# Kernel optimization log

Hardware: AMD Instinct MI355X
Metric: run time of the kernel (lower is better)

Reference implementation:

```python
import jax, jax.numpy as jnp
import numpy as np

# Supernet configuration (matches init_kwargs)
HIDDEN = [1024, 2048]
HEADS = [8, 16]
ABITS = [4, 8]
WBITS = [4, 8]
B, S = 4, 4096
MAX_IN = max(HIDDEN)            # 2048
MAX_OUT = max(HIDDEN)           # min(heads)*max(hidden)//min(heads) = 2048


def fake_quant(v, s, bit):
    """LSQ-style symmetric fake quantization with straight-through rounding."""
    qp = float(2 ** (bit - 1) - 1)
    qn = -float(2 ** (bit - 1))
    vs = jnp.clip(v / s, qn, qp)
    vq = vs + jax.lax.stop_gradient(jnp.round(vs) - vs)  # STE round
    return vq * s


def setup_inputs() -> dict:
    key = jax.random.key(0)
    k1, k2, k3, k4 = jax.random.split(key, 4)
    x = jax.random.normal(k1, (B, S, MAX_IN), jnp.float32)
    weights = jax.random.uniform(k2, (16,), jnp.float32)  # arch mixing coeffs
    W = jax.random.normal(k3, (MAX_OUT, MAX_IN), jnp.float32) * 0.02
    b = jax.random.normal(k4, (MAX_OUT,), jnp.float32) * 0.02
    # init_weight_scale: LSQ init 2*mean(|W|)/sqrt(Qp) per weight bitwidth
    w_scales = jnp.stack([2.0 * jnp.mean(jnp.abs(W)) / jnp.sqrt(float(2 ** (bit - 1) - 1))
                          for bit in WBITS])
    a_scales = jnp.ones((len(ABITS),), jnp.float32)
    return {"x": x, "weights": weights, "W": W, "b": b,
            "a_scales": a_scales, "w_scales": w_scales}


def reference(x, weights, W, b, a_scales, w_scales):
    # Non-argmax mixture path (reverse=False):
    # for each (hidden_i, heads_j, abit_m, wbit_n): slice W to
    # [out_dim, in_dim], zero-pad to [MAX_OUT, MAX_IN] (== masking, since
    # per-tensor fake-quant maps 0 -> 0), quantize, and weighted-accumulate.
    # Quantized x / W depend only on abit / wbit, so compute each once.
    qx = [fake_quant(x, a_scales[m], ABITS[m]) for m in range(len(ABITS))]   # [B,S,MAX_IN]
    qw = [fake_quant(W, w_scales[n], WBITS[n]) for n in range(len(WBITS))]  # [MAX_OUT,MAX_IN]
    out_idx = jnp.arange(MAX_OUT)
    in_idx = jnp.arange(MAX_IN)

    w_mix = jnp.zeros_like(W)
    x_mix = jnp.zeros_like(x)
    b_mix = jnp.zeros_like(b)
    k = 0
    for i, h in enumerate(HIDDEN):
        for j, nh in enumerate(HEADS):
            head_dim = h // nh
            out_dim = nh * head_dim  # == h when divisible
            in_dim = h
            wmask = (out_idx[:, None] < out_dim) & (in_idx[None, :] < in_dim)
            bmask = out_idx < out_dim
            for m in range(len(ABITS)):
                for n in range(len(WBITS)):
                    a = weights[k]
                    w_mix = w_mix + a * jnp.where(wmask, qw[n], 0.0)
                    x_mix = x_mix + a * qx[m]
                    b_mix = b_mix + a * jnp.where(bmask, b, 0.0)
                    k += 1
    # out = F.linear(x_mix, w_mix, b_mix)
    out = jnp.einsum('bsi,oi->bso', x_mix, w_mix) + b_mix
    return out
```

## Files before the change

### kernel.cpp

```cpp
#include <hip/hip_runtime.h>
#include <hip/hip_bf16.h>
#include <stdint.h>

#define MDIM 16384
#define NDIM 2048
#define KDIM 2048

typedef __attribute__((ext_vector_type(4))) float f32x4;
typedef __attribute__((ext_vector_type(8))) short s16x8;

__device__ __forceinline__ void gload_lds16(const __hip_bfloat16* g, void* l) {
    __builtin_amdgcn_global_load_lds(
        (const __attribute__((address_space(1))) void*)g,
        (__attribute__((address_space(3))) void*)l,
        16, 0, 0);
}

#define XBLKS 16384
#define WBLKS 2048

__global__ __launch_bounds__(256) void prep_all(
    const float* __restrict__ x, const float* __restrict__ weights,
    const float* __restrict__ W, const float* __restrict__ b,
    const float* __restrict__ a_scales, const float* __restrict__ w_scales,
    __hip_bfloat16* __restrict__ xq, __hip_bfloat16* __restrict__ wq,
    float* __restrict__ bm)
{
    const int blk = blockIdx.x;
    if (blk < XBLKS) {
        float A0 = 0.f, A1 = 0.f;
        #pragma unroll
        for (int k = 0; k < 16; ++k) {
            float w = weights[k];
            if (((k >> 1) & 1) == 0) A0 += w; else A1 += w;
        }
        const float s0 = a_scales[0], s1 = a_scales[1];
        const float r0 = 1.f / s0, r1 = 1.f / s1;

        size_t idx = ((size_t)blk * 256 + threadIdx.x) * 8;
        const f32x4* xv = (const f32x4*)(x + idx);
        f32x4 v0 = xv[0], v1 = xv[1];
        float vals[8] = {v0.x, v0.y, v0.z, v0.w, v1.x, v1.y, v1.z, v1.w};

        union { s16x8 v; __hip_bfloat16 h[8]; } u;
        #pragma unroll
        for (int j = 0; j < 8; ++j) {
            float q0 = rintf(fminf(fmaxf(vals[j] * r0, -8.f),   7.f)) * s0;
            float q1 = rintf(fminf(fmaxf(vals[j] * r1, -128.f), 127.f)) * s1;
            u.h[j] = __float2bfloat16(A0 * q0 + A1 * q1);
        }
        *(s16x8*)(xq + idx) = u.v;
    } else if (blk < XBLKS + WBLKS) {
        float c00 = weights[0] + weights[2]  + weights[4]  + weights[6];
        float c01 = weights[1] + weights[3]  + weights[5]  + weights[7];
        float c10 = weights[8] + weights[10] + weights[12] + weights[14];
        float c11 = weights[9] + weights[11] + weights[13] + weights[15];

        const float s0 = w_scales[0], s1 = w_scales[1];
        const float r0 = 1.f / s0, r1 = 1.f / s1;

        size_t idx = ((size_t)(blk - XBLKS) * 256 + threadIdx.x) * 8;
        const int o = (int)(idx >> 11);
        const int c = (int)(idx & 2047);
        const bool inner = (o < 1024) && (c < 1024);
        const float k0 = inner ? (c00 + c10) : c10;
        const float k1 = inner ? (c01 + c11) : c11;

        const f32x4* wv = (const f32x4*)(W + idx);
        f32x4 v0 = wv[0], v1 = wv[1];
        float vals[8] = {v0.x, v0.y, v0.z, v0.w, v1.x, v1.y, v1.z, v1.w};

        union { s16x8 v; __hip_bfloat16 h[8]; } u;
        #pragma unroll
        for (int j = 0; j < 8; ++j) {
            float q0 = rintf(fminf(fmaxf(vals[j] * r0, -8.f),   7.f)) * s0;
            float q1 = rintf(fminf(fmaxf(vals[j] * r1, -128.f), 127.f)) * s1;
            u.h[j] = __float2bfloat16(k0 * q0 + k1 * q1);
        }
        *(s16x8*)(wq + idx) = u.v;
    } else {
        int o = (blk - XBLKS - WBLKS) * 256 + threadIdx.x;
        if (o < NDIM) {
            float S1 = 0.f, S0 = 0.f;
            #pragma unroll
            for (int k = 0; k < 8; ++k)  S0 += weights[k];
            #pragma unroll
            for (int k = 8; k < 16; ++k) S1 += weights[k];
            bm[o] = b[o] * ((o < 1024) ? (S0 + S1) : S1);
        }
    }
}


#define NCH 64
#define ASLOT 16384
#define BREG  65536

#define MFMA(a, b, c) __builtin_amdgcn_mfma_f32_16x16x32_bf16((a), (b), (c), 0, 0, 0)

#define CHUNK(S, T)                                                          \
  {                                                                          \
    asm volatile("" ::: "memory");      \
    s16x8 af[8], bf[4];                                                      \
    _Pragma("unroll")                                                        \
    for (int m_ = 0; m_ < 8; ++m_)                                           \
      af[m_] = *(const s16x8*)(lds + (S) * ASLOT + aoff + m_ * 1024);        \
    _Pragma("unroll")                                                        \
    for (int n_ = 0; n_ < 4; ++n_)                                           \
      bf[n_] = *(const s16x8*)(lds + BREG + (S) * ASLOT + boff + n_ * 1024); \
    gload_lds16(As0 + kg * 32, lds + (T) * ASLOT + ldoff);                   \
    gload_lds16(As1 + kg * 32, lds + (T) * ASLOT + 8192 + ldoff);            \
    gload_lds16(Bs0 + kg * 32, lds + BREG + (T) * ASLOT + ldoff);            \
    gload_lds16(Bs1 + kg * 32, lds + BREG + (T) * ASLOT + 8192 + ldoff);     \
    kg = (kg + 1) & (NCH - 1);                                               \
    __builtin_amdgcn_s_setprio(1);                                           \
    _Pragma("unroll")                                                        \
    for (int m_ = 0; m_ < 8; ++m_) {                                         \
      acc[m_][0] = MFMA(af[m_], bf[0], acc[m_][0]);                          \
      acc[m_][1] = MFMA(af[m_], bf[1], acc[m_][1]);                          \
      acc[m_][2] = MFMA(af[m_], bf[2], acc[m_][2]);                          \
      acc[m_][3] = MFMA(af[m_], bf[3], acc[m_][3]);                          \
    }                                                                        \
    __builtin_amdgcn_s_setprio(0);                                           \
    asm volatile("s_waitcnt vmcnt(8)" ::: "memory");   \
    __builtin_amdgcn_s_barrier();                                            \
  }

__global__ __launch_bounds__(512, 2) void gemm256(
    const __hip_bfloat16* __restrict__ A,
    const __hip_bfloat16* __restrict__ B,
    const float* __restrict__ bias,
    float* __restrict__ C)
{
    __shared__ char lds[8 * ASLOT];

    const int tid  = threadIdx.x;
    const int lane = tid & 63;
    const int wid  = tid >> 6;
    const int wm   = wid >> 2;
    const int wn   = wid & 3;

    const int bid  = blockIdx.x;
    const int swz  = (bid & 7) * 64 + (bid >> 3);
    const int brow = (swz >> 3) * 256;
    const int bcol = (swz & 7) * 256;

    const int csw = (tid & 3) ^ ((tid >> 3) & 3);
    const __hip_bfloat16* As0 = A + (size_t)(brow + (tid >> 2)) * KDIM + csw * 8;
    const __hip_bfloat16* As1 = As0 + (size_t)128 * KDIM;
    const __hip_bfloat16* Bs0 = B + (size_t)(bcol + (tid >> 2)) * KDIM + csw * 8;
    const __hip_bfloat16* Bs1 = Bs0 + (size_t)128 * KDIM;
    const int ldoff = tid * 16;

    const int fr  = lane & 15;
    const int l16 = lane >> 4;
    const int xr  = (l16 ^ ((fr >> 1) & 3)) * 16;
    const int aoff = (wm * 128 + fr) * 64 + xr;
    const int boff = (wn * 64  + fr) * 64 + xr;

    f32x4 acc[8][4];
    #pragma unroll
    for (int m = 0; m < 8; ++m)
        #pragma unroll
        for (int n = 0; n < 4; ++n)
            acc[m][n] = (f32x4){0.f, 0.f, 0.f, 0.f};

    int kg = 3;

    #pragma unroll
    for (int q = 0; q < 3; ++q) {
        gload_lds16(As0 + q * 32, lds + q * ASLOT + ldoff);
        gload_lds16(As1 + q * 32, lds + q * ASLOT + 8192 + ldoff);
        gload_lds16(Bs0 + q * 32, lds + BREG + q * ASLOT + ldoff);
        gload_lds16(Bs1 + q * 32, lds + BREG + q * ASLOT + 8192 + ldoff);
    }
    asm volatile("s_waitcnt vmcnt(8)" ::: "memory");
    __builtin_amdgcn_s_barrier();

    #pragma unroll 1
    for (int it = 0; it < NCH / 4; ++it) {
        CHUNK(0, 3);
        CHUNK(1, 0);
        CHUNK(2, 1);
        CHUNK(3, 2);
    }
    asm volatile("s_waitcnt vmcnt(0) lgkmcnt(0)" ::: "memory");

    const int ccol0 = bcol + wn * 64 + fr;
    const int crow0 = brow + wm * 128 + l16 * 4;
    float bv[4];
    #pragma unroll
    for (int n = 0; n < 4; ++n) bv[n] = bias[ccol0 + n * 16];

    #pragma unroll
    for (int m = 0; m < 8; ++m) {
        #pragma unroll
        for (int j = 0; j < 4; ++j) {
            float* Crow = C + (size_t)(crow0 + m * 16 + j) * NDIM;
            #pragma unroll
            for (int n = 0; n < 4; ++n)
                Crow[ccol0 + n * 16] = acc[m][n][j] + bv[n];
        }
    }
}


extern "C" void kernel_launch(void* const* d_in, const int* in_sizes, int n_in,
                              void* d_out, int out_size, void* d_ws, size_t ws_size,
                              hipStream_t stream) {
    const float* x        = (const float*)d_in[0];
    const float* weights  = (const float*)d_in[1];
    const float* W        = (const float*)d_in[2];
    const float* b        = (const float*)d_in[3];
    const float* a_scales = (const float*)d_in[4];
    const float* w_scales = (const float*)d_in[5];
    float* out = (float*)d_out;

    __hip_bfloat16* xq = (__hip_bfloat16*)d_ws;
    __hip_bfloat16* wq = (__hip_bfloat16*)((char*)d_ws + 67108864);
    float*          bm = (float*)((char*)d_ws + 67108864 + 8388608);

    prep_all<<<dim3(XBLKS + WBLKS + 8), dim3(256), 0, stream>>>(
        x, weights, W, b, a_scales, w_scales, xq, wq, bm);
    gemm256<<<dim3((MDIM / 256) * (NDIM / 256)), dim3(512), 0, stream>>>(xq, wq, bm, out);
}
```

Baseline: 157.0 us.

## Process two K-chunks per barrier with a five-slot LDS ring

The GEMM main loop changes from a four-slot LDS ring with one barrier per 32-wide K chunk to a five-slot ring that handles two chunks per step. Each step reads the fragments for both chunks, issues two stages of global-to-LDS loads, and uses a single barrier, so there are half as many barriers and a longer span of MFMA work to cover load latency. The cost is more LDS (160KB per block) and twice as many fragment registers live at once, which may hurt occupancy at two blocks per CU. The slot rotation and the tail iterations are also more intricate and must cover exactly 64 chunks.

After: 190.0 us. 1.21x slower.

```diff
diff --git a/kernel.cpp b/kernel.cpp
--- a/kernel.cpp
+++ b/kernel.cpp
@@ -94,35 +94,47 @@
 
 #define NCH 64
 #define ASLOT 16384
-#define BREG  65536
+#define BREG  81920
 
 #define MFMA(a, b, c) __builtin_amdgcn_mfma_f32_16x16x32_bf16((a), (b), (c), 0, 0, 0)
 
-#define CHUNK(S, T)                                                          \
-  {                                                                          \
-    asm volatile("" ::: "memory");      \
-    s16x8 af[8], bf[4];                                                      \
+#define STAGE(KG, T)                                                         \
+    gload_lds16(As0 + (KG) * 32, lds + (T) * ASLOT + ldoff);                 \
+    gload_lds16(As1 + (KG) * 32, lds + (T) * ASLOT + 8192 + ldoff);          \
+    gload_lds16(Bs0 + (KG) * 32, lds + BREG + (T) * ASLOT + ldoff);          \
+    gload_lds16(Bs1 + (KG) * 32, lds + BREG + (T) * ASLOT + 8192 + ldoff);
+
+#define RD(AF, BF, S)                                                        \
     _Pragma("unroll")                                                        \
     for (int m_ = 0; m_ < 8; ++m_)                                           \
-      af[m_] = *(const s16x8*)(lds + (S) * ASLOT + aoff + m_ * 1024);        \
+      AF[m_] = *(const s16x8*)(lds + (S) * ASLOT + aoff + m_ * 1024);        \
     _Pragma("unroll")                                                        \
     for (int n_ = 0; n_ < 4; ++n_)                                           \
-      bf[n_] = *(const s16x8*)(lds + BREG + (S) * ASLOT + boff + n_ * 1024); \
-    gload_lds16(As0 + kg * 32, lds + (T) * ASLOT + ldoff);                   \
-    gload_lds16(As1 + kg * 32, lds + (T) * ASLOT + 8192 + ldoff);            \
-    gload_lds16(Bs0 + kg * 32, lds + BREG + (T) * ASLOT + ldoff);            \
-    gload_lds16(Bs1 + kg * 32, lds + BREG + (T) * ASLOT + 8192 + ldoff);     \
-    kg = (kg + 1) & (NCH - 1);                                               \
+      BF[n_] = *(const s16x8*)(lds + BREG + (S) * ASLOT + boff + n_ * 1024);
+
+#define MM(AF, BF)                                                           \
     __builtin_amdgcn_s_setprio(1);                                           \
     _Pragma("unroll")                                                        \
     for (int m_ = 0; m_ < 8; ++m_) {                                         \
-      acc[m_][0] = MFMA(af[m_], bf[0], acc[m_][0]);                          \
-      acc[m_][1] = MFMA(af[m_], bf[1], acc[m_][1]);                          \
-      acc[m_][2] = MFMA(af[m_], bf[2], acc[m_][2]);                          \
-      acc[m_][3] = MFMA(af[m_], bf[3], acc[m_][3]);                          \
+      acc[m_][0] = MFMA(AF[m_], BF[0], acc[m_][0]);                          \
+      acc[m_][1] = MFMA(AF[m_], BF[1], acc[m_][1]);                          \
+      acc[m_][2] = MFMA(AF[m_], BF[2], acc[m_][2]);                          \
+      acc[m_][3] = MFMA(AF[m_], BF[3], acc[m_][3]);                          \
     }                                                                        \
-    __builtin_amdgcn_s_setprio(0);                                           \
-    asm volatile("s_waitcnt vmcnt(8)" ::: "memory");   \
+    __builtin_amdgcn_s_setprio(0);
+
+#define STEP(S0, S1, T0, T1)                                                 \
+  {                                                                          \
+    asm volatile("" ::: "memory");                                           \
+    s16x8 af0[8], bf0[4], af1[8], bf1[4];                                    \
+    RD(af0, bf0, S0);                                                        \
+    STAGE(kg, T0);                                                           \
+    RD(af1, bf1, S1);               \
+    MM(af0, bf0);                                                            \
+    STAGE(kg + 1, T1);                                                       \
+    MM(af1, bf1);                                                            \
+    kg = (kg + 2) & (NCH - 1);                                               \
+    asm volatile("s_waitcnt vmcnt(4)" ::: "memory");                         \
     __builtin_amdgcn_s_barrier();                                            \
   }
 
@@ -132,7 +144,7 @@
     const float* __restrict__ bias,
     float* __restrict__ C)
 {
-    __shared__ char lds[8 * ASLOT];
+    __shared__ char lds[10 * ASLOT];
 
     const int tid  = threadIdx.x;
     const int lane = tid & 63;
@@ -168,22 +180,20 @@
     int kg = 3;
 
     #pragma unroll
-    for (int q = 0; q < 3; ++q) {
-        gload_lds16(As0 + q * 32, lds + q * ASLOT + ldoff);
-        gload_lds16(As1 + q * 32, lds + q * ASLOT + 8192 + ldoff);
-        gload_lds16(Bs0 + q * 32, lds + BREG + q * ASLOT + ldoff);
-        gload_lds16(Bs1 + q * 32, lds + BREG + q * ASLOT + 8192 + ldoff);
+    for (int q = 0; q < 3; ++q) { STAGE(q, q); }
+    asm volatile("s_waitcnt vmcnt(4)" ::: "memory");
+    __builtin_amdgcn_s_barrier();
+
+    #pragma unroll 1
+    for (int it = 0; it < 6; ++it) {
+        STEP(0, 1, 3, 4);
+        STEP(2, 3, 0, 1);
+        STEP(4, 0, 2, 3);
+        STEP(1, 2, 4, 0);
+        STEP(3, 4, 1, 2);
     }
-    asm volatile("s_waitcnt vmcnt(8)" ::: "memory");
-    __builtin_amdgcn_s_barrier();
-
-    #pragma unroll 1
-    for (int it = 0; it < NCH / 4; ++it) {
-        CHUNK(0, 3);
-        CHUNK(1, 0);
-        CHUNK(2, 1);
-        CHUNK(3, 2);
-    }
+    STEP(0, 1, 3, 4);
+    STEP(2, 3, 0, 1);
     asm volatile("s_waitcnt vmcnt(0) lgkmcnt(0)" ::: "memory");
 
     const int ccol0 = bcol + wn * 64 + fr;
```
